# Performance work log

Measured on AMD Instinct MI355X. Metric: run time of the kernel, lower is better.

The kernel has to match this reference:

```python
import jax, jax.numpy as jnp
import numpy as np
import math

B, L, DF = 1024, 96, 5
D_MODEL, D_FF, N_HEADS = 256, 1024, 8
C_OUT, MA, FACTOR = 5, 25, 3
E_LAYERS, D_LAYERS, EXT = 2, 2, 20


def moving_mean(x, k):
    # torch moving_avg: replicate-pad (k-1)//2 on each side, AvgPool1d(k, stride=1)
    p = (k - 1) // 2
    xp = jnp.concatenate([jnp.repeat(x[:, :1], p, axis=1), x, jnp.repeat(x[:, -1:], p, axis=1)], axis=1)
    cs = jnp.cumsum(xp, axis=1)
    cs = jnp.concatenate([jnp.zeros_like(cs[:, :1]), cs], axis=1)
    return (cs[:, k:] - cs[:, :-k]) / k


def series_decomp(x, k):
    m = moving_mean(x, k)
    return x - m, m


def circ_conv3(x, W):
    # Conv1d(kernel=3, padding=1, padding_mode='circular', bias=False); x (B,T,C), W (O,C,3)
    xp = jnp.pad(x, ((0, 0), (1, 1), (0, 0)), mode='wrap')
    win = jnp.stack([xp[:, :-2], xp[:, 1:-1], xp[:, 2:]], axis=-1)  # (B,T,C,3)
    return jnp.einsum('btct,oct->bto'.replace('btct', 'blct').replace('bto', 'blo'), win, W)


def my_layernorm(x, g, b):
    # LayerNorm over last dim, then subtract per-(batch,channel) seasonal bias (mean over time)
    mu = x.mean(-1, keepdims=True)
    var = ((x - mu) ** 2).mean(-1, keepdims=True)
    xh = (x - mu) / jnp.sqrt(var + 1e-5) * g + b
    return xh - xh.mean(axis=1, keepdims=True)


def time_delay_agg(values, corr):
    # inference-mode time delay aggregation; values, corr: (B,H,E,Lv)
    Bv, H, E, Lv = values.shape
    top_k = int(FACTOR * math.log(Lv))
    mean_value = corr.mean(axis=(1, 2))              # (B,Lv)
    weights, delay = jax.lax.top_k(mean_value, top_k)  # (B,k)
    tmp_corr = jax.nn.softmax(weights, axis=-1)
    ar = jnp.arange(Lv)

    def body(acc, wd):
        w, d = wd                                    # (B,), (B,) int32
        idx = (ar[None, :] + d[:, None]) % Lv        # circular roll == gather on doubled values
        pattern = jnp.take_along_axis(values, idx[:, None, None, :], axis=-1)
        return acc + pattern * w[:, None, None, None], None

    acc, _ = jax.lax.scan(body, jnp.zeros_like(values), (tmp_corr.T, delay.T))
    return acc


def auto_correlation(q, k, v):
    # q (B,Lq,H,E); k,v (B,S,H,E)
    Bq, Lq, H, E = q.shape
    S = v.shape[1]
    if Lq > S:
        pad = jnp.zeros((Bq, Lq - S, H, E), q.dtype)
        k = jnp.concatenate([k, pad], axis=1)
        v = jnp.concatenate([v, pad], axis=1)
    else:
        k, v = k[:, :Lq], v[:, :Lq]
    qf = jnp.fft.rfft(q.transpose(0, 2, 3, 1), axis=-1)
    kf = jnp.fft.rfft(k.transpose(0, 2, 3, 1), axis=-1)
    corr = jnp.fft.irfft(qf * jnp.conj(kf), n=Lq, axis=-1)  # (B,H,E,Lq)
    V = time_delay_agg(v.transpose(0, 2, 3, 1), corr)
    return V.transpose(0, 3, 1, 2)


def ac_layer(xq, xkv, Wq, bq, Wk, bk, Wv, bv, Wo, bo):
    Bq, Lq, _ = xq.shape
    S = xkv.shape[1]
    q = (xq @ Wq.T + bq).reshape(Bq, Lq, N_HEADS, -1)
    k = (xkv @ Wk.T + bk).reshape(Bq, S, N_HEADS, -1)
    v = (xkv @ Wv.T + bv).reshape(Bq, S, N_HEADS, -1)
    V = auto_correlation(q, k, v).reshape(Bq, Lq, -1)
    return V @ Wo.T + bo


def setup_inputs() -> dict:
    ks = iter(jax.random.split(jax.random.key(0), 64))

    def rn(shape, s=0.05):
        return jax.random.normal(next(ks), shape, jnp.float32) * s

    dm, E, D = D_MODEL, E_LAYERS, D_LAYERS
    inp = {'x': jax.random.normal(next(ks), (B, L, DF), jnp.float32)}
    inp['we_enc'] = rn((dm, DF, 3), 0.3)
    inp['we_dec'] = rn((dm, DF, 3), 0.3)
    for w in ('Wq', 'Wk', 'Wv', 'Wo'):
        inp['enc_' + w] = rn((E, dm, dm))
        inp['enc_b' + w[1]] = rn((E, dm))
    inp['enc_W1'] = rn((E, D_FF, dm))
    inp['enc_W2'] = rn((E, dm, D_FF))
    inp['enc_ln_g'] = jnp.ones((dm,), jnp.float32)
    inp['enc_ln_b'] = jnp.zeros((dm,), jnp.float32)
    for p in ('s', 'c'):
        for w in ('Wq', 'Wk', 'Wv', 'Wo'):
            inp['dec_' + p + w] = rn((D, dm, dm))
            inp['dec_' + p + 'b' + w[1]] = rn((D, dm))
    inp['dec_W1'] = rn((D, D_FF, dm))
    inp['dec_W2'] = rn((D, dm, D_FF))
    inp['dec_Wt'] = rn((D, C_OUT, dm, 3), 0.3)
    inp['dec_ln_g'] = jnp.ones((dm,), jnp.float32)
    inp['dec_ln_b'] = jnp.zeros((dm,), jnp.float32)
    inp['proj_W'] = rn((C_OUT, dm), 0.3)
    inp['proj_b'] = jnp.zeros((C_OUT,), jnp.float32)
    inp['bn_g'] = jnp.ones((EXT,), jnp.float32)
    inp['bn_b'] = jnp.zeros((EXT,), jnp.float32)
    inp['bn_rm'] = jnp.zeros((EXT,), jnp.float32)
    inp['bn_rv'] = jnp.ones((EXT,), jnp.float32)
    inp['fc_W'] = rn((1, EXT), 0.3)
    inp['fc_b'] = jnp.zeros((1,), jnp.float32)
    return inp


def reference(x, we_enc, we_dec,
              enc_Wq, enc_bq, enc_Wk, enc_bk, enc_Wv, enc_bv, enc_Wo, enc_bo,
              enc_W1, enc_W2, enc_ln_g, enc_ln_b,
              dec_sWq, dec_sbq, dec_sWk, dec_sbk, dec_sWv, dec_sbv, dec_sWo, dec_sbo,
              dec_cWq, dec_cbq, dec_cWk, dec_cbk, dec_cWv, dec_cbv, dec_cWo, dec_cbo,
              dec_W1, dec_W2, dec_Wt, dec_ln_g, dec_ln_b,
              proj_W, proj_b, bn_g, bn_b, bn_rm, bn_rv, fc_W, fc_b):
    mean = jnp.tile(x.mean(axis=1, keepdims=True), (1, EXT, 1))
    seasonal_init, trend_init = series_decomp(x, MA)
    trend_init = jnp.concatenate([trend_init, mean], axis=1)            # (B, L+EXT, DF)
    seasonal_init = jnp.pad(seasonal_init, ((0, 0), (EXT, 0), (0, 0)))  # 20 zero steps in front
    # encoder
    enc = circ_conv3(x, we_enc)  # DataEmbedding_wo_pos (dropout = identity in eval)
    for i in range(E_LAYERS):
        a = ac_layer(enc, enc, enc_Wq[i], enc_bq[i], enc_Wk[i], enc_bk[i],
                     enc_Wv[i], enc_bv[i], enc_Wo[i], enc_bo[i])
        h, _ = series_decomp(enc + a, MA)
        y = jax.nn.relu(h @ enc_W1[i].T) @ enc_W2[i].T  # 1x1 convs, bias=False
        enc, _ = series_decomp(h + y, MA)
    enc = my_layernorm(enc, enc_ln_g, enc_ln_b)
    # decoder
    dec = circ_conv3(seasonal_init, we_dec)
    trend = trend_init
    for i in range(D_LAYERS):
        a = ac_layer(dec, dec, dec_sWq[i], dec_sbq[i], dec_sWk[i], dec_sbk[i],
                     dec_sWv[i], dec_sbv[i], dec_sWo[i], dec_sbo[i])
        dec, t1 = series_decomp(dec + a, MA)
        a = ac_layer(dec, enc, dec_cWq[i], dec_cbq[i], dec_cWk[i], dec_cbk[i],
                     dec_cWv[i], dec_cbv[i], dec_cWo[i], dec_cbo[i])
        dec, t2 = series_decomp(dec + a, MA)
        y = jax.nn.relu(dec @ dec_W1[i].T) @ dec_W2[i].T
        dec, t3 = series_decomp(dec + y, MA)
        trend = trend + circ_conv3(t1 + t2 + t3, dec_Wt[i])
    dec = my_layernorm(dec, dec_ln_g, dec_ln_b)
    seasonal = dec @ proj_W.T + proj_b          # (B, L+EXT, C_OUT)
    seasonal = jnp.tile(seasonal, (1, 1, 4))    # (B, L+EXT, 20)
    out = jnp.tile(trend, (1, 1, 4)) + seasonal  # trend tiled to 20 channels (see notes)
    last = out[:, -1, :]                         # (B, 20)
    h = (last - bn_rm) / jnp.sqrt(bn_rv + 1e-5) * bn_g + bn_b  # BatchNorm1d eval
    return (h @ fc_W.T + fc_b)[:, 0]
```

## Files before the change

### kernel.cpp

```cpp
#include <hip/hip_runtime.h>
#include <hip/hip_bf16.h>
#include <cstdint>
#include <cstddef>

#define B_   1024
#define LE   96
#define LD   116
#define DM   256
#define DFF  1024

typedef __attribute__((ext_vector_type(8))) short bf16x8;
typedef __attribute__((ext_vector_type(4))) float f32x4;

static __device__ __forceinline__ unsigned short f2b(float f) {
  __hip_bfloat16 h = __float2bfloat16(f);
  return *reinterpret_cast<unsigned short*>(&h);
}
static __device__ __forceinline__ float asf(unsigned int u) { return __uint_as_float(u); }

static __device__ __forceinline__ void split8(float4 a, float4 b, uint4& h4, uint4& l4) {
  float f[8] = {a.x, a.y, a.z, a.w, b.x, b.y, b.z, b.w};
  unsigned int hp[4], lp[4];
#pragma unroll
  for (int j = 0; j < 4; ++j) {
    unsigned short h0 = f2b(f[2 * j]);
    unsigned short h1 = f2b(f[2 * j + 1]);
    float r0 = f[2 * j]     - asf((unsigned int)h0 << 16);
    float r1 = f[2 * j + 1] - asf((unsigned int)h1 << 16);
    hp[j] = (unsigned int)h0 | ((unsigned int)h1 << 16);
    lp[j] = (unsigned int)f2b(r0) | ((unsigned int)f2b(r1) << 16);
  }
  h4 = make_uint4(hp[0], hp[1], hp[2], hp[3]);
  l4 = make_uint4(lp[0], lp[1], lp[2], lp[3]);
}

typedef const __attribute__((address_space(1))) void* gas_ptr;
typedef __attribute__((address_space(3))) void* las_ptr;
static __device__ __forceinline__ void gload16(const void* g, void* l) {
  __builtin_amdgcn_global_load_lds((gas_ptr)g, (las_ptr)l, 16, 0, 0);
}

#define NE_ ((size_t)B_ * LE * DM)
#define ND_ ((size_t)B_ * LD * DM)
#define NS_ ((size_t)B_ * LD * 5)
#define NW_ ((size_t)B_ * 16)
#define WBF_ 3670016

static constexpr size_t o_enc   = 0;
static constexpr size_t o_dec   = o_enc   + NE_ * 4;
static constexpr size_t o_q     = o_dec   + ND_ * 4;
static constexpr size_t o_kbuf  = o_q     + ND_ * 4;
static constexpr size_t o_spad  = o_kbuf  + ND_ * 4;
static constexpr size_t o_trend = o_spad  + NS_ * 4;
static constexpr size_t o_wtop  = o_trend + NS_ * 4;
static constexpr size_t o_dtop  = o_wtop  + NW_ * 4;
static constexpr size_t o_whi   = o_dtop  + NW_ * 4;
static constexpr size_t o_wlo   = o_whi   + (size_t)WBF_ * 2;
static constexpr size_t WS_TOTAL = o_wlo  + (size_t)WBF_ * 2;

__device__ __align__(256) unsigned char g_ws[WS_TOTAL];

static constexpr size_t wq_e = 0, wk_e = 131072, wv_e = 262144, wo_e = 393216;
static constexpr size_t w1_e = 524288, w2_e = 1048576;
static constexpr size_t swq_e = 1572864, swk_e = 1703936, swv_e = 1835008, swo_e = 1966080;
static constexpr size_t cwq_e = 2097152, cwk_e = 2228224, cwv_e = 2359296, cwo_e = 2490368;
static constexpr size_t dw1_e = 2621440, dw2_e = 3145728;

__global__ __launch_bounds__(256)
void k_cast_split(const float* __restrict__ in, unsigned short* __restrict__ hi,
                  unsigned short* __restrict__ lo, int n) {
  int i = (blockIdx.x * 256 + threadIdx.x) * 4;
  if (i < n) {
    float4 v = *(const float4*)(in + i);
    unsigned int hp[2], lp[2];
    float f[4] = {v.x, v.y, v.z, v.w};
#pragma unroll
    for (int j = 0; j < 2; ++j) {
      unsigned short h0 = f2b(f[2 * j]);
      unsigned short h1 = f2b(f[2 * j + 1]);
      float r0 = f[2 * j]     - asf((unsigned int)h0 << 16);
      float r1 = f[2 * j + 1] - asf((unsigned int)h1 << 16);
      hp[j] = (unsigned int)h0 | ((unsigned int)h1 << 16);
      lp[j] = (unsigned int)f2b(r0) | ((unsigned int)f2b(r1) << 16);
    }
    *(uint2*)(hi + i) = make_uint2(hp[0], hp[1]);
    *(uint2*)(lo + i) = make_uint2(lp[0], lp[1]);
  }
}

__global__ __launch_bounds__(128)
void k_pre(const float* __restrict__ x, float* __restrict__ spad, float* __restrict__ trend) {
  int b = blockIdx.x;
  __shared__ float xs[LE * 5];
  __shared__ float mx[5];
  const float* xb = x + (size_t)b * LE * 5;
  for (int i = threadIdx.x; i < LE * 5; i += 128) xs[i] = xb[i];
  __syncthreads();
  if (threadIdx.x < 5) {
    float s = 0.f;
    for (int t = 0; t < LE; ++t) s += xs[t * 5 + threadIdx.x];
    mx[threadIdx.x] = s * (1.f / 96.f);
  }
  __syncthreads();
  float* spb = spad + (size_t)b * LD * 5;
  float* trb = trend + (size_t)b * LD * 5;
  for (int i = threadIdx.x; i < LE * 5; i += 128) {
    int t = i / 5, c = i % 5;
    float s = 0.f;
    for (int d = -12; d <= 12; ++d) {
      int tt = t + d; tt = tt < 0 ? 0 : (tt > LE - 1 ? LE - 1 : tt);
      s += xs[tt * 5 + c];
    }
    float m = s * (1.f / 25.f);
    trb[t * 5 + c] = m;
    spb[(t + 20) * 5 + c] = xs[i] - m;
  }
  for (int i = threadIdx.x; i < 20 * 5; i += 128) {
    int t = i / 5, c = i % 5;
    spb[t * 5 + c] = 0.f;
    trb[(LE + t) * 5 + c] = mx[c];
  }
}

__global__ __launch_bounds__(256)
void k_conv3(const float* __restrict__ xin, const float* __restrict__ W,
             float* __restrict__ out, int L) {
  int b = blockIdx.x, o = threadIdx.x;
  __shared__ float xs[LD * 5];
  const float* xb = xin + (size_t)b * L * 5;
  for (int i = o; i < L * 5; i += 256) xs[i] = xb[i];
  __syncthreads();
  float w[15];
#pragma unroll
  for (int j = 0; j < 15; ++j) w[j] = W[o * 15 + j];
  float* ob = out + (size_t)b * L * DM;
  for (int l = 0; l < L; ++l) {
    int lm = (l == 0) ? L - 1 : l - 1;
    int lp = (l == L - 1) ? 0 : l + 1;
    float acc = 0.f;
#pragma unroll
    for (int c = 0; c < 5; ++c)
      acc += xs[lm * 5 + c] * w[c * 3] + xs[l * 5 + c] * w[c * 3 + 1] + xs[lp * 5 + c] * w[c * 3 + 2];
    ob[(size_t)l * DM + o] = acc;
  }
}

template <bool RELU>
__global__ __launch_bounds__(256)
void k_gemm_split(const float* __restrict__ X,
                  const unsigned short* __restrict__ Whi, const unsigned short* __restrict__ Wlo,
                  const float* __restrict__ bias, float* __restrict__ C,
                  int M, int N, int K) {
  __shared__ __align__(16) unsigned short Xh[4096], Xl[4096], Wh[4096], Wl[4096];
  const int nwg = gridDim.x, bid = blockIdx.x;
  const int wg = (bid & 7) * (nwg >> 3) + (bid >> 3);
  const int NT = N >> 7;
  const int mt = wg / NT, nt = wg % NT;
  const int m0 = mt << 7, n0 = nt << 7;
  const int tid = threadIdx.x, lane = tid & 63, wv = tid >> 6;
  const int wm = (wv >> 1) << 6, wn = (wv & 1) << 6;

  f32x4 acc[4][4];
#pragma unroll
  for (int i = 0; i < 4; ++i)
#pragma unroll
    for (int j = 0; j < 4; ++j) acc[i][j] = (f32x4){0.f, 0.f, 0.f, 0.f};

  const int r0 = tid >> 2,        ls0 = (tid & 3) ^ ((r0 >> 1) & 3);
  const int r1 = 64 + (tid >> 2), ls1 = (tid & 3) ^ ((r1 >> 1) & 3);
  const unsigned short* wh0 = Whi + (size_t)(n0 + r0) * K + (ls0 << 3);
  const unsigned short* wh1 = Whi + (size_t)(n0 + r1) * K + (ls1 << 3);
  const unsigned short* wl0 = Wlo + (size_t)(n0 + r0) * K + (ls0 << 3);
  const unsigned short* wl1 = Wlo + (size_t)(n0 + r1) * K + (ls1 << 3);
  unsigned short* lwh0 = Wh + ((tid & ~63) << 3);
  unsigned short* lwh1 = Wh + 2048 + ((tid & ~63) << 3);
  unsigned short* lwl0 = Wl + ((tid & ~63) << 3);
  unsigned short* lwl1 = Wl + 2048 + ((tid & ~63) << 3);

  const int xrow0 = tid >> 2, xpart = tid & 3;
  const int xrow1 = 64 + xrow0;
  const float* xp0 = X + (size_t)(m0 + xrow0) * K + (xpart << 3);
  const float* xp1 = X + (size_t)(m0 + xrow1) * K + (xpart << 3);
  const int xph0 = xpart ^ ((xrow0 >> 1) & 3);
  const int xph1 = xpart ^ ((xrow1 >> 1) & 3);
  unsigned short* xh0d = Xh + xrow0 * 32 + (xph0 << 3);
  unsigned short* xl0d = Xl + xrow0 * 32 + (xph0 << 3);
  unsigned short* xh1d = Xh + xrow1 * 32 + (xph1 << 3);
  unsigned short* xl1d = Xl + xrow1 * 32 + (xph1 << 3);

  for (int k0 = 0; k0 < K; k0 += 32) {
    gload16(wh0 + k0, lwh0);
    gload16(wh1 + k0, lwh1);
    gload16(wl0 + k0, lwl0);
    gload16(wl1 + k0, lwl1);
    {
      float4 a0 = *(const float4*)(xp0 + k0);
      float4 b0 = *(const float4*)(xp0 + k0 + 4);
      float4 a1 = *(const float4*)(xp1 + k0);
      float4 b1 = *(const float4*)(xp1 + k0 + 4);
      uint4 h, l;
      split8(a0, b0, h, l);
      *(uint4*)xh0d = h; *(uint4*)xl0d = l;
      split8(a1, b1, h, l);
      *(uint4*)xh1d = h; *(uint4*)xl1d = l;
    }
    __syncthreads();
    bf16x8 ah[4], al[4], bh[4], bl[4];
#pragma unroll
    for (int i = 0; i < 4; ++i) {
      int ra = wm + i * 16 + (lane & 15);
      int sa = (lane >> 4) ^ ((ra >> 1) & 3);
      ah[i] = *(const bf16x8*)(Xh + ra * 32 + (sa << 3));
      al[i] = *(const bf16x8*)(Xl + ra * 32 + (sa << 3));
      int rb = wn + i * 16 + (lane & 15);
      int sb = (lane >> 4) ^ ((rb >> 1) & 3);
      bh[i] = *(const bf16x8*)(Wh + rb * 32 + (sb << 3));
      bl[i] = *(const bf16x8*)(Wl + rb * 32 + (sb << 3));
    }
#pragma unroll
    for (int i = 0; i < 4; ++i)
#pragma unroll
      for (int j = 0; j < 4; ++j) {
        acc[i][j] = __builtin_amdgcn_mfma_f32_16x16x32_bf16(ah[i], bh[j], acc[i][j], 0, 0, 0);
        acc[i][j] = __builtin_amdgcn_mfma_f32_16x16x32_bf16(al[i], bh[j], acc[i][j], 0, 0, 0);
        acc[i][j] = __builtin_amdgcn_mfma_f32_16x16x32_bf16(ah[i], bl[j], acc[i][j], 0, 0, 0);
      }
    __syncthreads();
  }

  const int col_base = n0 + wn + (lane & 15);
  const int row_base = m0 + wm + ((lane >> 4) << 2);
#pragma unroll
  for (int j = 0; j < 4; ++j) {
    int col = col_base + j * 16;
    float bv = bias ? bias[col] : 0.f;
#pragma unroll
    for (int i = 0; i < 4; ++i) {
      int rb2 = row_base + i * 16;
#pragma unroll
      for (int q = 0; q < 4; ++q) {
        float o = acc[i][j][q] + bv;
        if (RELU) o = fmaxf(o, 0.f);
        C[(size_t)(rb2 + q) * N + col] = o;
      }
    }
  }
}

__global__ __launch_bounds__(256)
void k_corr_split(const float* __restrict__ Q, const float* __restrict__ Kp,
                  float* __restrict__ wout, int* __restrict__ dout,
                  int L, int S, int TK) {
  __shared__ __align__(16) unsigned char smem[65536];
  unsigned short* qh = (unsigned short*)smem;
  unsigned short* ql = qh + 8192;
  unsigned short* kh = ql + 8192;
  unsigned short* kl = kh + 8192;
  float* G = (float*)smem;
  int b = blockIdx.x, tid = threadIdx.x, lane = tid & 63, wv = tid >> 6;
  int wm = (wv >> 1) << 6, wn = (wv & 1) << 6;
  const float* Qb = Q + (size_t)b * L * DM;
  const float* Kb = Kp + (size_t)b * S * DM;
  f32x4 acc[4][4];
#pragma unroll
  for (int i = 0; i < 4; ++i)
#pragma unroll
    for (int j = 0; j < 4; ++j) acc[i][j] = (f32x4){0.f, 0.f, 0.f, 0.f};

  for (int c0 = 0; c0 < DM; c0 += 64) {
#pragma unroll
    for (int u = 0; u < 4; ++u) {
      int seg = (u << 8) + tid;
      int row = seg >> 3, ps = seg & 7;
      int phys = ps ^ (row & 7);
      uint4 h = make_uint4(0u, 0u, 0u, 0u), l = make_uint4(0u, 0u, 0u, 0u);
      if (row < L) {
        float4 a = *(const float4*)(Qb + (size_t)row * DM + c0 + (ps << 3));
        float4 c = *(const float4*)(Qb + (size_t)row * DM + c0 + (ps << 3) + 4);
        split8(a, c, h, l);
      }
      *(uint4*)(qh + row * 64 + (phys << 3)) = h;
      *(uint4*)(ql + row * 64 + (phys << 3)) = l;
      h = make_uint4(0u, 0u, 0u, 0u); l = make_uint4(0u, 0u, 0u, 0u);
      if (row < S) {
        float4 a = *(const float4*)(Kb + (size_t)row * DM + c0 + (ps << 3));
        float4 c = *(const float4*)(Kb + (size_t)row * DM + c0 + (ps << 3) + 4);
        split8(a, c, h, l);
      }
      *(uint4*)(kh + row * 64 + (phys << 3)) = h;
      *(uint4*)(kl + row * 64 + (phys << 3)) = l;
    }
    __syncthreads();
#pragma unroll
    for (int ks = 0; ks < 2; ++ks) {
      bf16x8 aqh[4], aql[4], bkh[4], bkl[4];
#pragma unroll
      for (int i = 0; i < 4; ++i) {
        int ra = wm + i * 16 + (lane & 15);
        int sa = ((ks << 2) + (lane >> 4)) ^ (ra & 7);
        aqh[i] = *(const bf16x8*)(qh + ra * 64 + (sa << 3));
        aql[i] = *(const bf16x8*)(ql + ra * 64 + (sa << 3));
        int rb = wn + i * 16 + (lane & 15);
        int sb = ((ks << 2) + (lane >> 4)) ^ (rb & 7);
        bkh[i] = *(const bf16x8*)(kh + rb * 64 + (sb << 3));
        bkl[i] = *(const bf16x8*)(kl + rb * 64 + (sb << 3));
      }
#pragma unroll
      for (int i = 0; i < 4; ++i)
#pragma unroll
        for (int j = 0; j < 4; ++j) {
          acc[i][j] = __builtin_amdgcn_mfma_f32_16x16x32_bf16(aqh[i], bkh[j], acc[i][j], 0, 0, 0);
          acc[i][j] = __builtin_amdgcn_mfma_f32_16x16x32_bf16(aql[i], bkh[j], acc[i][j], 0, 0, 0);
          acc[i][j] = __builtin_amdgcn_mfma_f32_16x16x32_bf16(aqh[i], bkl[j], acc[i][j], 0, 0, 0);
        }
    }
    __syncthreads();
  }
#pragma unroll
  for (int i = 0; i < 4; ++i)
#pragma unroll
    for (int j = 0; j < 4; ++j)
#pragma unroll
      for (int q = 0; q < 4; ++q)
        G[(wm + i * 16 + ((lane >> 4) << 2) + q) * 128 + wn + j * 16 + (lane & 15)] = acc[i][j][q];
  __syncthreads();
  float s = 0.f;
  if (tid < L) {
    for (int t = 0; t < L; ++t) {
      int r = t - tid; if (r < 0) r += L;
      s += G[t * 128 + r];
    }
    s *= (1.f / 256.f);
  }
  __syncthreads();

  float* vals = (float*)smem;
  float* rv   = vals + 128;
  int*   ri   = (int*)(rv + 128);
  float* selv = (float*)(ri + 128);
  int*   seli = (int*)(selv + 16);
  if (tid < 128) vals[tid] = (tid < L) ? s : -3e38f;
  __syncthreads();
  for (int it = 0; it < TK; ++it) {
    if (tid < 128) { rv[tid] = vals[tid]; ri[tid] = tid; }
    __syncthreads();
    for (int off = 64; off >= 1; off >>= 1) {
      if (tid < off) {
        float v2 = rv[tid + off]; int i2 = ri[tid + off];
        if (v2 > rv[tid] || (v2 == rv[tid] && i2 < ri[tid])) { rv[tid] = v2; ri[tid] = i2; }
      }
      __syncthreads();
    }
    if (tid == 0) { selv[it] = rv[0]; seli[it] = ri[0]; vals[ri[0]] = -3e38f; }
    __syncthreads();
  }
  if (tid == 0) {
    float mxv = selv[0];
    float e[16]; float sum = 0.f;
    for (int j = 0; j < TK; ++j) { e[j] = expf(selv[j] - mxv); sum += e[j]; }
    float inv = 1.f / sum;
    for (int j = 0; j < TK; ++j) {
      wout[(size_t)b * 16 + j] = e[j] * inv;
      dout[(size_t)b * 16 + j] = seli[j];
    }
  }
}

__global__ __launch_bounds__(256)
void k_gather4(const float* __restrict__ V, const float* __restrict__ wtop,
               const int* __restrict__ dtop, float* __restrict__ out,
               int L, int S, int TK, int G8) {
  int p = blockIdx.x;
  int xcd = p & 7, q8 = p >> 3;
  int lg = q8 % G8;
  int b = ((q8 / G8) << 3) + xcd;
  __shared__ float wsm[16];
  __shared__ int   dsm[16];
  if (threadIdx.x < TK) {
    wsm[threadIdx.x] = wtop[(size_t)b * 16 + threadIdx.x];
    dsm[threadIdx.x] = dtop[(size_t)b * 16 + threadIdx.x];
  }
  __syncthreads();
  int wv = threadIdx.x >> 6, lane = threadIdx.x & 63;
  int c4 = lane << 2;
  const float* Vb = V + (size_t)b * S * DM + c4;
  float* ob = out + (size_t)b * L * DM + c4;
#pragma unroll
  for (int u = 0; u < 2; ++u) {
    int l = (lg << 3) + (wv << 1) + u;
    if (l < L) {
      float ax = 0.f, ay = 0.f, az = 0.f, aw = 0.f;
      for (int j = 0; j < TK; ++j) {
        int r = l + dsm[j]; if (r >= L) r -= L;
        if (r < S) {
          float4 v = *(const float4*)(Vb + (size_t)r * DM);
          float w = wsm[j];
          ax += w * v.x; ay += w * v.y; az += w * v.z; aw += w * v.w;
        }
      }
      float4 o; o.x = ax; o.y = ay; o.z = az; o.w = aw;
      *(float4*)(ob + (size_t)l * DM) = o;
    }
  }
}

template <int MOUT>
__global__ __launch_bounds__(128)
void k_decomp(const float* __restrict__ X, const float* __restrict__ Y,
              float* __restrict__ out, float* __restrict__ mout, int L) {
  int b = blockIdx.x >> 1, half = blockIdx.x & 1;
  __shared__ float tmp[LD * 128];
  size_t base = (size_t)b * L * DM + half * 128;
  for (int i = threadIdx.x; i < L * 128; i += 128) {
    int t = i >> 7, cc = i & 127;
    size_t gi = base + (size_t)t * DM + cc;
    tmp[i] = X[gi] + Y[gi];
  }
  __syncthreads();
  int tid = threadIdx.x;
  float s = 0.f;
  for (int d = -12; d <= 12; ++d) { int t2 = d < 0 ? 0 : d; s += tmp[t2 * 128 + tid]; }
  for (int t = 0; t < L; ++t) {
    float m = s * (1.f / 25.f);
    size_t gi = base + (size_t)t * DM + tid;
    out[gi] = tmp[t * 128 + tid] - m;
    if (MOUT) mout[gi] = m;
    int ai = t + 13; if (ai > L - 1) ai = L - 1;
    int si = t - 12; if (si < 0) si = 0;
    s += tmp[ai * 128 + tid] - tmp[si * 128 + tid];
  }
}

__global__ __launch_bounds__(256)
void k_lnorm(const float* __restrict__ X, const float* __restrict__ g,
             float* __restrict__ out, int L) {
  int b = blockIdx.x;
  __shared__ float mu_s[LD], inv_s[LD];
  size_t base = (size_t)b * L * DM;
  int wv = threadIdx.x >> 6, lane = threadIdx.x & 63;
  for (int t = wv; t < L; t += 4) {
    float s = 0.f, s2 = 0.f;
#pragma unroll
    for (int qd = 0; qd < 4; ++qd) {
      float val = X[base + (size_t)t * DM + lane + 64 * qd];
      s += val; s2 += val * val;
    }
    for (int off = 32; off; off >>= 1) { s += __shfl_xor(s, off); s2 += __shfl_xor(s2, off); }
    if (lane == 0) {
      float mu = s * (1.f / 256.f);
      mu_s[t] = mu;
      inv_s[t] = rsqrtf(s2 * (1.f / 256.f) - mu * mu + 1e-5f);
    }
  }
  __syncthreads();
  int c = threadIdx.x;
  float gc = g[c];
  float sm = 0.f;
  for (int t = 0; t < L; ++t) sm += (X[base + (size_t)t * DM + c] - mu_s[t]) * inv_s[t];
  float mn = sm / (float)L;
  for (int t = 0; t < L; ++t) {
    float xn = (X[base + (size_t)t * DM + c] - mu_s[t]) * inv_s[t];
    out[base + (size_t)t * DM + c] = gc * (xn - mn);
  }
}

__global__ __launch_bounds__(256)
void k_trendconv(const float* __restrict__ T, const float* __restrict__ Wt,
                 float* __restrict__ trend, int L) {
  int b = blockIdx.x;
  int tid = threadIdx.x, wv = tid >> 6, lane = tid & 63;
  int c0 = lane << 2;
  float w[5][3][4];
#pragma unroll
  for (int o = 0; o < 5; ++o)
#pragma unroll
    for (int k = 0; k < 4; ++k) {
      w[o][0][k] = Wt[o * 768 + (c0 + k) * 3 + 0];
      w[o][1][k] = Wt[o * 768 + (c0 + k) * 3 + 1];
      w[o][2][k] = Wt[o * 768 + (c0 + k) * 3 + 2];
    }
  size_t base = (size_t)b * L * DM;
  for (int l = wv; l < L; l += 4) {
    int lm = (l == 0) ? L - 1 : l - 1;
    int lp = (l == L - 1) ? 0 : l + 1;
    float4 xm = *(const float4*)(T + base + (size_t)lm * DM + c0);
    float4 x0 = *(const float4*)(T + base + (size_t)l  * DM + c0);
    float4 xp = *(const float4*)(T + base + (size_t)lp * DM + c0);
    float fm[4] = {xm.x, xm.y, xm.z, xm.w};
    float f0[4] = {x0.x, x0.y, x0.z, x0.w};
    float fp[4] = {xp.x, xp.y, xp.z, xp.w};
    float acc[5];
#pragma unroll
    for (int o = 0; o < 5; ++o) {
      float a = 0.f;
#pragma unroll
      for (int k = 0; k < 4; ++k)
        a += fm[k] * w[o][0][k] + f0[k] * w[o][1][k] + fp[k] * w[o][2][k];
      acc[o] = a;
    }
#pragma unroll
    for (int off = 32; off; off >>= 1)
#pragma unroll
      for (int o = 0; o < 5; ++o) acc[o] += __shfl_xor(acc[o], off);
    if (lane == 0) {
#pragma unroll
      for (int o = 0; o < 5; ++o)
        trend[((size_t)b * L + l) * 5 + o] += acc[o];
    }
  }
}

__global__ __launch_bounds__(256)
void k_final(const float* __restrict__ dec, const float* __restrict__ trend,
             const float* __restrict__ projW, const float* __restrict__ projb,
             const float* __restrict__ bng, const float* __restrict__ bnb,
             const float* __restrict__ bnrm, const float* __restrict__ bnrv,
             const float* __restrict__ fcW, const float* __restrict__ fcb,
             float* __restrict__ outp) {
  int b = blockIdx.x, c = threadIdx.x;
  __shared__ float red[5][256];
  float xv = dec[((size_t)b * LD + (LD - 1)) * DM + c];
#pragma unroll
  for (int o = 0; o < 5; ++o) red[o][c] = xv * projW[o * 256 + c];
  __syncthreads();
  for (int off = 128; off >= 1; off >>= 1) {
    if (c < off) {
#pragma unroll
      for (int o = 0; o < 5; ++o) red[o][c] += red[o][c + off];
    }
    __syncthreads();
  }
  if (c == 0) {
    float acc = fcb[0];
    for (int j = 0; j < 20; ++j) {
      int m5 = j % 5;
      float last = trend[((size_t)b * LD + (LD - 1)) * 5 + m5] + red[m5][0] + projb[m5];
      float h = (last - bnrm[j]) * rsqrtf(bnrv[j] + 1e-5f) * bng[j] + bnb[j];
      acc += h * fcW[j];
    }
    outp[b] = acc;
  }
}

extern "C" void kernel_launch(void* const* d_in, const int* in_sizes, int n_in,
                              void* d_out, int out_size, void* d_ws, size_t ws_size,
                              hipStream_t stream) {
  const float* x      = (const float*)d_in[0];
  const float* we_enc = (const float*)d_in[1];
  const float* we_dec = (const float*)d_in[2];
  const float* enc_Wq = (const float*)d_in[3];
  const float* enc_bq = (const float*)d_in[4];
  const float* enc_Wk = (const float*)d_in[5];
  const float* enc_bk = (const float*)d_in[6];
  const float* enc_Wv = (const float*)d_in[7];
  const float* enc_bv = (const float*)d_in[8];
  const float* enc_Wo = (const float*)d_in[9];
  const float* enc_bo = (const float*)d_in[10];
  const float* enc_W1 = (const float*)d_in[11];
  const float* enc_W2 = (const float*)d_in[12];
  const float* enc_g  = (const float*)d_in[13];
  const float* sWq = (const float*)d_in[15]; const float* sbq = (const float*)d_in[16];
  const float* sWk = (const float*)d_in[17]; const float* sbk = (const float*)d_in[18];
  const float* sWv = (const float*)d_in[19]; const float* sbv = (const float*)d_in[20];
  const float* sWo = (const float*)d_in[21]; const float* sbo = (const float*)d_in[22];
  const float* cWq = (const float*)d_in[23]; const float* cbq = (const float*)d_in[24];
  const float* cWk = (const float*)d_in[25]; const float* cbk = (const float*)d_in[26];
  const float* cWv = (const float*)d_in[27]; const float* cbv = (const float*)d_in[28];
  const float* cWo = (const float*)d_in[29]; const float* cbo = (const float*)d_in[30];
  const float* dW1 = (const float*)d_in[31]; const float* dW2 = (const float*)d_in[32];
  const float* dWt = (const float*)d_in[33];
  const float* dec_g  = (const float*)d_in[34];
  const float* projW = (const float*)d_in[36]; const float* projb = (const float*)d_in[37];
  const float* bng = (const float*)d_in[38]; const float* bnb = (const float*)d_in[39];
  const float* bnrm = (const float*)d_in[40]; const float* bnrv = (const float*)d_in[41];
  const float* fcW = (const float*)d_in[42]; const float* fcb = (const float*)d_in[43];
  (void)in_sizes; (void)n_in; (void)out_size; (void)d_ws; (void)ws_size;
  float* outp = (float*)d_out;

  void* symaddr = nullptr;
  if (hipGetSymbolAddress(&symaddr, HIP_SYMBOL(g_ws)) != hipSuccess || !symaddr) return;
  unsigned char* base = (unsigned char*)symaddr;
  float* enc   = (float*)(base + o_enc);
  float* dec   = (float*)(base + o_dec);
  float* q     = (float*)(base + o_q);
  float* kbuf  = (float*)(base + o_kbuf);
  float* spad  = (float*)(base + o_spad);
  float* trend = (float*)(base + o_trend);
  float* wtop  = (float*)(base + o_wtop);
  int*   dtop  = (int*)(base + o_dtop);
  unsigned short* whi = (unsigned short*)(base + o_whi);
  unsigned short* wlo = (unsigned short*)(base + o_wlo);

  const int ME = B_ * LE;
  const int MD = B_ * LD;

  auto cast = [&](const float* s, size_t off, int n) {
    k_cast_split<<<n / 1024, 256, 0, stream>>>(s, whi + off, wlo + off, n);
  };
  cast(enc_Wq, wq_e, 131072);  cast(enc_Wk, wk_e, 131072);
  cast(enc_Wv, wv_e, 131072);  cast(enc_Wo, wo_e, 131072);
  cast(enc_W1, w1_e, 524288);  cast(enc_W2, w2_e, 524288);
  cast(sWq, swq_e, 131072);    cast(sWk, swk_e, 131072);
  cast(sWv, swv_e, 131072);    cast(sWo, swo_e, 131072);
  cast(cWq, cwq_e, 131072);    cast(cWk, cwk_e, 131072);
  cast(cWv, cwv_e, 131072);    cast(cWo, cwo_e, 131072);
  cast(dW1, dw1_e, 524288);    cast(dW2, dw2_e, 524288);

  auto gemm = [&](const float* X, size_t woff, const float* bias, float* C,
                  int M, int N, int K, bool relu) {
    int nwg = (M >> 7) * (N >> 7);
    if (relu) k_gemm_split<true ><<<nwg, 256, 0, stream>>>(X, whi + woff, wlo + woff, bias, C, M, N, K);
    else      k_gemm_split<false><<<nwg, 256, 0, stream>>>(X, whi + woff, wlo + woff, bias, C, M, N, K);
  };
  auto ffn = [&](const float* xb, int M, size_t w1, size_t w2) {
    int done = 0;
    while (done < M) {
      int mc = (M - done < 29696) ? (M - done) : 29696;
      gemm(xb + (size_t)done * DM, w1, nullptr, q, mc, DFF, DM, true);
      gemm(q, w2, nullptr, kbuf + (size_t)done * DM, mc, DM, DFF, false);
      done += mc;
    }
  };
  auto attn = [&](const float* src_q, int Lq, const float* src_kv, int S,
                  size_t wq, size_t wk, size_t wv2, size_t wo2,
                  const float* bq, const float* bk, const float* bv, const float* bo, int TK) {
    int Mq = B_ * Lq, Ms = B_ * S;
    int G8 = (Lq + 7) >> 3;
    gemm(src_q,  wq,  bq, q,    Mq, DM, DM, false);
    gemm(src_kv, wk,  bk, kbuf, Ms, DM, DM, false);
    k_corr_split<<<B_, 256, 0, stream>>>(q, kbuf, wtop, dtop, Lq, S, TK);
    gemm(src_kv, wv2, bv, q, Ms, DM, DM, false);
    k_gather4<<<B_ * G8, 256, 0, stream>>>(q, wtop, dtop, kbuf, Lq, S, TK, G8);
    gemm(kbuf, wo2, bo, q, Mq, DM, DM, false);
  };

  k_pre<<<B_, 128, 0, stream>>>(x, spad, trend);
  k_conv3<<<B_, 256, 0, stream>>>(x, we_enc, enc, LE);
  k_conv3<<<B_, 256, 0, stream>>>(spad, we_dec, dec, LD);

  for (int i = 0; i < 2; ++i) {
    size_t wofs = (size_t)i * 65536, b_ = (size_t)i * DM, f1 = (size_t)i * 262144;
    attn(enc, LE, enc, LE, wq_e + wofs, wk_e + wofs, wv_e + wofs, wo_e + wofs,
         enc_bq + b_, enc_bk + b_, enc_bv + b_, enc_bo + b_, 13);
    k_decomp<0><<<2 * B_, 128, 0, stream>>>(enc, q, enc, nullptr, LE);
    ffn(enc, ME, w1_e + f1, w2_e + f1);
    k_decomp<0><<<2 * B_, 128, 0, stream>>>(enc, kbuf, enc, nullptr, LE);
  }
  k_lnorm<<<B_, 256, 0, stream>>>(enc, enc_g, enc, LE);

  for (int i = 0; i < 2; ++i) {
    size_t wofs = (size_t)i * 65536, b_ = (size_t)i * DM, f1 = (size_t)i * 262144;
    const float* Wt_i = dWt + (size_t)i * 5 * DM * 3;
    attn(dec, LD, dec, LD, swq_e + wofs, swk_e + wofs, swv_e + wofs, swo_e + wofs,
         sbq + b_, sbk + b_, sbv + b_, sbo + b_, 14);
    k_decomp<1><<<2 * B_, 128, 0, stream>>>(dec, q, dec, kbuf, LD);
    k_trendconv<<<B_, 256, 0, stream>>>(kbuf, Wt_i, trend, LD);
    attn(dec, LD, enc, LE, cwq_e + wofs, cwk_e + wofs, cwv_e + wofs, cwo_e + wofs,
         cbq + b_, cbk + b_, cbv + b_, cbo + b_, 14);
    k_decomp<1><<<2 * B_, 128, 0, stream>>>(dec, q, dec, kbuf, LD);
    k_trendconv<<<B_, 256, 0, stream>>>(kbuf, Wt_i, trend, LD);
    ffn(dec, MD, dw1_e + f1, dw2_e + f1);
    k_decomp<1><<<2 * B_, 128, 0, stream>>>(dec, kbuf, dec, q, LD);
    k_trendconv<<<B_, 256, 0, stream>>>(q, Wt_i, trend, LD);
  }
  k_lnorm<<<B_, 256, 0, stream>>>(dec, dec_g, dec, LD);

  k_final<<<B_, 256, 0, stream>>>(dec, trend, projW, projb, bng, bnb, bnrm, bnrv, fcW, fcb, outp);
}
```

Baseline: 6.185 ms.

## Fuse Q/K/V projections into one wide GEMM and split decomp across quarter-channel blocks

Reorders the bf16 hi/lo weight buffers so each layer's Q, K and V (or K and V for cross attention) are contiguous, and concatenates their biases. This lets a single GEMM with N=768 (or 512) produce all projections into a strided qkv buffer. The correlation and gather kernels take row strides so they can read straight from that buffer. Separately, the series-decomposition kernel now uses four blocks per batch with 64 channels each and two time halves per block, giving more parallelism and less shared memory per block. The cost is a larger workspace and extra small setup launches.

```diff
diff --git a/kernel.cpp b/kernel.cpp
--- a/kernel.cpp
+++ b/kernel.cpp
@@ -50,21 +50,20 @@
 static constexpr size_t o_dec   = o_enc   + NE_ * 4;
 static constexpr size_t o_q     = o_dec   + ND_ * 4;
 static constexpr size_t o_kbuf  = o_q     + ND_ * 4;
-static constexpr size_t o_spad  = o_kbuf  + ND_ * 4;
+static constexpr size_t o_qkv   = o_kbuf  + ND_ * 4;
+static constexpr size_t o_spad  = o_qkv   + ND_ * 12;
 static constexpr size_t o_trend = o_spad  + NS_ * 4;
 static constexpr size_t o_wtop  = o_trend + NS_ * 4;
 static constexpr size_t o_dtop  = o_wtop  + NW_ * 4;
-static constexpr size_t o_whi   = o_dtop  + NW_ * 4;
+static constexpr size_t o_bias  = o_dtop  + NW_ * 4;
+static constexpr size_t o_whi   = o_bias  + 6 * 768 * 4;
 static constexpr size_t o_wlo   = o_whi   + (size_t)WBF_ * 2;
 static constexpr size_t WS_TOTAL = o_wlo  + (size_t)WBF_ * 2;
 
 __device__ __align__(256) unsigned char g_ws[WS_TOTAL];
 
-static constexpr size_t wq_e = 0, wk_e = 131072, wv_e = 262144, wo_e = 393216;
-static constexpr size_t w1_e = 524288, w2_e = 1048576;
-static constexpr size_t swq_e = 1572864, swk_e = 1703936, swv_e = 1835008, swo_e = 1966080;
-static constexpr size_t cwq_e = 2097152, cwk_e = 2228224, cwv_e = 2359296, cwo_e = 2490368;
-static constexpr size_t dw1_e = 2621440, dw2_e = 3145728;
+static __host__ __device__ constexpr size_t enc_base(int i) { return (size_t)i * 786432; }
+static __host__ __device__ constexpr size_t dec_base(int i) { return 1572864 + (size_t)i * 1048576; }
 
 __global__ __launch_bounds__(256)
 void k_cast_split(const float* __restrict__ in, unsigned short* __restrict__ hi,
@@ -86,6 +85,15 @@
     *(uint2*)(hi + i) = make_uint2(hp[0], hp[1]);
     *(uint2*)(lo + i) = make_uint2(lp[0], lp[1]);
   }
+}
+
+__global__ __launch_bounds__(256)
+void k_cat3(const float* __restrict__ a, const float* __restrict__ b,
+            const float* __restrict__ c, float* __restrict__ dst) {
+  int t = threadIdx.x;
+  dst[t] = a[t];
+  dst[256 + t] = b[t];
+  if (c) dst[512 + t] = c[t];
 }
 
 __global__ __launch_bounds__(128)
@@ -248,7 +256,7 @@
 }
 
 __global__ __launch_bounds__(256)
-void k_corr_split(const float* __restrict__ Q, const float* __restrict__ Kp,
+void k_corr_split(const float* __restrict__ Q, int sq, const float* __restrict__ Kp, int sk,
                   float* __restrict__ wout, int* __restrict__ dout,
                   int L, int S, int TK) {
   __shared__ __align__(16) unsigned char smem[65536];
@@ -259,8 +267,8 @@
   float* G = (float*)smem;
   int b = blockIdx.x, tid = threadIdx.x, lane = tid & 63, wv = tid >> 6;
   int wm = (wv >> 1) << 6, wn = (wv & 1) << 6;
-  const float* Qb = Q + (size_t)b * L * DM;
-  const float* Kb = Kp + (size_t)b * S * DM;
+  const float* Qb = Q + (size_t)b * L * sq;
+  const float* Kb = Kp + (size_t)b * S * sk;
   f32x4 acc[4][4];
 #pragma unroll
   for (int i = 0; i < 4; ++i)
@@ -275,16 +283,16 @@
       int phys = ps ^ (row & 7);
       uint4 h = make_uint4(0u, 0u, 0u, 0u), l = make_uint4(0u, 0u, 0u, 0u);
       if (row < L) {
-        float4 a = *(const float4*)(Qb + (size_t)row * DM + c0 + (ps << 3));
-        float4 c = *(const float4*)(Qb + (size_t)row * DM + c0 + (ps << 3) + 4);
+        float4 a = *(const float4*)(Qb + (size_t)row * sq + c0 + (ps << 3));
+        float4 c = *(const float4*)(Qb + (size_t)row * sq + c0 + (ps << 3) + 4);
         split8(a, c, h, l);
       }
       *(uint4*)(qh + row * 64 + (phys << 3)) = h;
       *(uint4*)(ql + row * 64 + (phys << 3)) = l;
       h = make_uint4(0u, 0u, 0u, 0u); l = make_uint4(0u, 0u, 0u, 0u);
       if (row < S) {
-        float4 a = *(const float4*)(Kb + (size_t)row * DM + c0 + (ps << 3));
-        float4 c = *(const float4*)(Kb + (size_t)row * DM + c0 + (ps << 3) + 4);
+        float4 a = *(const float4*)(Kb + (size_t)row * sk + c0 + (ps << 3));
+        float4 c = *(const float4*)(Kb + (size_t)row * sk + c0 + (ps << 3) + 4);
         split8(a, c, h, l);
       }
       *(uint4*)(kh + row * 64 + (phys << 3)) = h;
@@ -367,7 +375,7 @@
 }
 
 __global__ __launch_bounds__(256)
-void k_gather4(const float* __restrict__ V, const float* __restrict__ wtop,
+void k_gather4(const float* __restrict__ V, int sv, const float* __restrict__ wtop,
                const int* __restrict__ dtop, float* __restrict__ out,
                int L, int S, int TK, int G8) {
   int p = blockIdx.x;
@@ -383,7 +391,7 @@
   __syncthreads();
   int wv = threadIdx.x >> 6, lane = threadIdx.x & 63;
   int c4 = lane << 2;
-  const float* Vb = V + (size_t)b * S * DM + c4;
+  const float* Vb = V + (size_t)b * S * sv + c4;
   float* ob = out + (size_t)b * L * DM + c4;
 #pragma unroll
   for (int u = 0; u < 2; ++u) {
@@ -393,7 +401,7 @@
       for (int j = 0; j < TK; ++j) {
         int r = l + dsm[j]; if (r >= L) r -= L;
         if (r < S) {
-          float4 v = *(const float4*)(Vb + (size_t)r * DM);
+          float4 v = *(const float4*)(Vb + (size_t)r * sv);
           float w = wsm[j];
           ax += w * v.x; ay += w * v.y; az += w * v.z; aw += w * v.w;
         }
@@ -408,26 +416,31 @@
 __global__ __launch_bounds__(128)
 void k_decomp(const float* __restrict__ X, const float* __restrict__ Y,
               float* __restrict__ out, float* __restrict__ mout, int L) {
-  int b = blockIdx.x >> 1, half = blockIdx.x & 1;
-  __shared__ float tmp[LD * 128];
-  size_t base = (size_t)b * L * DM + half * 128;
-  for (int i = threadIdx.x; i < L * 128; i += 128) {
-    int t = i >> 7, cc = i & 127;
+  int b = blockIdx.x >> 2, qd = blockIdx.x & 3;
+  __shared__ float tmp[LD * 64];
+  size_t base = (size_t)b * L * DM + qd * 64;
+  for (int i = threadIdx.x; i < L * 64; i += 128) {
+    int t = i >> 6, cc = i & 63;
     size_t gi = base + (size_t)t * DM + cc;
     tmp[i] = X[gi] + Y[gi];
   }
   __syncthreads();
-  int tid = threadIdx.x;
+  int c = threadIdx.x & 63, th = threadIdx.x >> 6;
+  int half = L >> 1;
+  int t0 = th * half, t1 = t0 + half;
   float s = 0.f;
-  for (int d = -12; d <= 12; ++d) { int t2 = d < 0 ? 0 : d; s += tmp[t2 * 128 + tid]; }
-  for (int t = 0; t < L; ++t) {
+  for (int d = -12; d <= 12; ++d) {
+    int t2 = t0 + d; t2 = t2 < 0 ? 0 : (t2 > L - 1 ? L - 1 : t2);
+    s += tmp[t2 * 64 + c];
+  }
+  for (int t = t0; t < t1; ++t) {
     float m = s * (1.f / 25.f);
-    size_t gi = base + (size_t)t * DM + tid;
-    out[gi] = tmp[t * 128 + tid] - m;
+    size_t gi = base + (size_t)t * DM + c;
+    out[gi] = tmp[t * 64 + c] - m;
     if (MOUT) mout[gi] = m;
     int ai = t + 13; if (ai > L - 1) ai = L - 1;
     int si = t - 12; if (si < 0) si = 0;
-    s += tmp[ai * 128 + tid] - tmp[si * 128 + tid];
+    s += tmp[ai * 64 + c] - tmp[si * 64 + c];
   }
 }
 
@@ -584,10 +597,12 @@
   float* dec   = (float*)(base + o_dec);
   float* q     = (float*)(base + o_q);
   float* kbuf  = (float*)(base + o_kbuf);
+  float* qkv   = (float*)(base + o_qkv);
   float* spad  = (float*)(base + o_spad);
   float* trend = (float*)(base + o_trend);
   float* wtop  = (float*)(base + o_wtop);
   int*   dtop  = (int*)(base + o_dtop);
+  float* biasb = (float*)(base + o_bias);
   unsigned short* whi = (unsigned short*)(base + o_whi);
   unsigned short* wlo = (unsigned short*)(base + o_wlo);
 
@@ -597,14 +612,22 @@
   auto cast = [&](const float* s, size_t off, int n) {
     k_cast_split<<<n / 1024, 256, 0, stream>>>(s, whi + off, wlo + off, n);
   };
-  cast(enc_Wq, wq_e, 131072);  cast(enc_Wk, wk_e, 131072);
-  cast(enc_Wv, wv_e, 131072);  cast(enc_Wo, wo_e, 131072);
-  cast(enc_W1, w1_e, 524288);  cast(enc_W2, w2_e, 524288);
-  cast(sWq, swq_e, 131072);    cast(sWk, swk_e, 131072);
-  cast(sWv, swv_e, 131072);    cast(sWo, swo_e, 131072);
-  cast(cWq, cwq_e, 131072);    cast(cWk, cwk_e, 131072);
-  cast(cWv, cwv_e, 131072);    cast(cWo, cwo_e, 131072);
-  cast(dW1, dw1_e, 524288);    cast(dW2, dw2_e, 524288);
+  for (int i = 0; i < 2; ++i) {
+    size_t e = enc_base(i), d = dec_base(i);
+    size_t wq = (size_t)i * 65536, wf = (size_t)i * 262144;
+    cast(enc_Wq + wq, e + 0, 65536);       cast(enc_Wk + wq, e + 65536, 65536);
+    cast(enc_Wv + wq, e + 131072, 65536);  cast(enc_Wo + wq, e + 196608, 65536);
+    cast(enc_W1 + wf, e + 262144, 262144); cast(enc_W2 + wf, e + 524288, 262144);
+    cast(sWq + wq, d + 0, 65536);          cast(sWk + wq, d + 65536, 65536);
+    cast(sWv + wq, d + 131072, 65536);     cast(sWo + wq, d + 196608, 65536);
+    cast(cWq + wq, d + 262144, 65536);     cast(cWk + wq, d + 327680, 65536);
+    cast(cWv + wq, d + 393216, 65536);     cast(cWo + wq, d + 458752, 65536);
+    cast(dW1 + wf, d + 524288, 262144);    cast(dW2 + wf, d + 786432, 262144);
+    size_t b_ = (size_t)i * DM;
+    k_cat3<<<1, 256, 0, stream>>>(enc_bq + b_, enc_bk + b_, enc_bv + b_, biasb + (size_t)i * 768);
+    k_cat3<<<1, 256, 0, stream>>>(sbq + b_, sbk + b_, sbv + b_, biasb + (size_t)(2 + i) * 768);
+    k_cat3<<<1, 256, 0, stream>>>(cbk + b_, cbv + b_, nullptr, biasb + (size_t)(4 + i) * 768);
+  }
 
   auto gemm = [&](const float* X, size_t woff, const float* bias, float* C,
                   int M, int N, int K, bool relu) {
@@ -621,17 +644,23 @@
       done += mc;
     }
   };
-  auto attn = [&](const float* src_q, int Lq, const float* src_kv, int S,
-                  size_t wq, size_t wk, size_t wv2, size_t wo2,
-                  const float* bq, const float* bk, const float* bv, const float* bo, int TK) {
-    int Mq = B_ * Lq, Ms = B_ * S;
+  auto attn_self = [&](const float* src, int Lq, size_t wqkv, size_t wo2,
+                       const float* biasr, const float* bo, int TK) {
+    int M = B_ * Lq;
     int G8 = (Lq + 7) >> 3;
-    gemm(src_q,  wq,  bq, q,    Mq, DM, DM, false);
-    gemm(src_kv, wk,  bk, kbuf, Ms, DM, DM, false);
-    k_corr_split<<<B_, 256, 0, stream>>>(q, kbuf, wtop, dtop, Lq, S, TK);
-    gemm(src_kv, wv2, bv, q, Ms, DM, DM, false);
-    k_gather4<<<B_ * G8, 256, 0, stream>>>(q, wtop, dtop, kbuf, Lq, S, TK, G8);
-    gemm(kbuf, wo2, bo, q, Mq, DM, DM, false);
+    gemm(src, wqkv, biasr, qkv, M, 768, DM, false);
+    k_corr_split<<<B_, 256, 0, stream>>>(qkv, 768, qkv + 256, 768, wtop, dtop, Lq, Lq, TK);
+    k_gather4<<<B_ * G8, 256, 0, stream>>>(qkv + 512, 768, wtop, dtop, kbuf, Lq, Lq, TK, G8);
+    gemm(kbuf, wo2, bo, q, M, DM, DM, false);
+  };
+  auto attn_cross = [&](size_t wq2, size_t wkv, size_t wo2, const float* bq,
+                        const float* biasr, const float* bo, int TK) {
+    int G8 = (LD + 7) >> 3;
+    gemm(dec, wq2, bq, q, MD, DM, DM, false);
+    gemm(enc, wkv, biasr, qkv, ME, 512, DM, false);
+    k_corr_split<<<B_, 256, 0, stream>>>(q, 256, qkv, 512, wtop, dtop, LD, LE, TK);
+    k_gather4<<<B_ * G8, 256, 0, stream>>>(qkv + 256, 512, wtop, dtop, kbuf, LD, LE, TK, G8);
+    gemm(kbuf, wo2, bo, q, MD, DM, DM, false);
   };
 
   k_pre<<<B_, 128, 0, stream>>>(x, spad, trend);
@@ -639,28 +668,25 @@
   k_conv3<<<B_, 256, 0, stream>>>(spad, we_dec, dec, LD);
 
   for (int i = 0; i < 2; ++i) {
-    size_t wofs = (size_t)i * 65536, b_ = (size_t)i * DM, f1 = (size_t)i * 262144;
-    attn(enc, LE, enc, LE, wq_e + wofs, wk_e + wofs, wv_e + wofs, wo_e + wofs,
-         enc_bq + b_, enc_bk + b_, enc_bv + b_, enc_bo + b_, 13);
-    k_decomp<0><<<2 * B_, 128, 0, stream>>>(enc, q, enc, nullptr, LE);
-    ffn(enc, ME, w1_e + f1, w2_e + f1);
-    k_decomp<0><<<2 * B_, 128, 0, stream>>>(enc, kbuf, enc, nullptr, LE);
+    size_t e = enc_base(i), b_ = (size_t)i * DM;
+    attn_self(enc, LE, e + 0, e + 196608, biasb + (size_t)i * 768, enc_bo + b_, 13);
+    k_decomp<0><<<4 * B_, 128, 0, stream>>>(enc, q, enc, nullptr, LE);
+    ffn(enc, ME, e + 262144, e + 524288);
+    k_decomp<0><<<4 * B_, 128, 0, stream>>>(enc, kbuf, enc, nullptr, LE);
   }
   k_lnorm<<<B_, 256, 0, stream>>>(enc, enc_g, enc, LE);
 
   for (int i = 0; i < 2; ++i) {
-    size_t wofs = (size_t)i * 65536, b_ = (size_t)i * DM, f1 = (size_t)i * 262144;
+    size_t d = dec_base(i), b_ = (size_t)i * DM;
     const float* Wt_i = dWt + (size_t)i * 5 * DM * 3;
-    attn(dec, LD, dec, LD, swq_e + wofs, swk_e + wofs, swv_e + wofs, swo_e + wofs,
-         sbq + b_, sbk + b_, sbv + b_, sbo + b_, 14);
-    k_decomp<1><<<2 * B_, 128, 0, stream>>>(dec, q, dec, kbuf, LD);
+    attn_self(dec, LD, d + 0, d + 196608, biasb + (size_t)(2 + i) * 768, sbo + b_, 14);
+    k_decomp<1><<<4 * B_, 128, 0, stream>>>(dec, q, dec, kbuf, LD);
     k_trendconv<<<B_, 256, 0, stream>>>(kbuf, Wt_i, trend, LD);
-    attn(dec, LD, enc, LE, cwq_e + wofs, cwk_e + wofs, cwv_e + wofs, cwo_e + wofs,
-         cbq + b_, cbk + b_, cbv + b_, cbo + b_, 14);
-    k_decomp<1><<<2 * B_, 128, 0, stream>>>(dec, q, dec, kbuf, LD);
+    attn_cross(d + 262144, d + 327680, d + 458752, cbq + b_, biasb + (size_t)(4 + i) * 768, cbo + b_, 14);
+    k_decomp<1><<<4 * B_, 128, 0, stream>>>(dec, q, dec, kbuf, LD);
     k_trendconv<<<B_, 256, 0, stream>>>(kbuf, Wt_i, trend, LD);
-    ffn(dec, MD, dw1_e + f1, dw2_e + f1);
-    k_decomp<1><<<2 * B_, 128, 0, stream>>>(dec, kbuf, dec, q, LD);
+    ffn(dec, MD, d + 524288, d + 786432);
+    k_decomp<1><<<4 * B_, 128, 0, stream>>>(dec, kbuf, dec, q, LD);
     k_trendconv<<<B_, 256, 0, stream>>>(q, Wt_i, trend, LD);
   }
   k_lnorm<<<B_, 256, 0, stream>>>(dec, dec_g, dec, LD);
```

Result: no change. 6.296 ms (+1.8%).
